# Optimization experiments

Hardware: AMD Instinct MI355X
Metric: run time of the kernel (lower is better)

Reference implementation:

```python
import jax, jax.numpy as jnp
import numpy as np

C = 256      # n_embd
H = 16       # n_head
HS = C // H  # head_size = 16
B = 64
T = 256      # <= block_size
LN_EPS = 1e-5


def _layer_norm(x, g, b):
    mu = jnp.mean(x, axis=-1, keepdims=True)
    var = jnp.mean((x - mu) ** 2, axis=-1, keepdims=True)
    return (x - mu) * jax.lax.rsqrt(var + LN_EPS) * g + b


def setup_inputs() -> dict:
    key = jax.random.key(0)
    ks = jax.random.split(key, 10)
    s_in = 1.0 / np.sqrt(C)
    s_ff = 1.0 / np.sqrt(4 * C)
    return {
        "x": jax.random.normal(ks[0], (B, T, C), dtype=jnp.float32),
        # per-head Q/K/V weights, stacked: [H, C, HS] (no bias, as in Head)
        "Wq": jax.random.normal(ks[1], (H, C, HS), dtype=jnp.float32) * s_in,
        "Wk": jax.random.normal(ks[2], (H, C, HS), dtype=jnp.float32) * s_in,
        "Wv": jax.random.normal(ks[3], (H, C, HS), dtype=jnp.float32) * s_in,
        "Wp": jax.random.normal(ks[4], (C, C), dtype=jnp.float32) * s_in,
        "bp": jnp.zeros((C,), dtype=jnp.float32),
        "W1": jax.random.normal(ks[5], (C, 4 * C), dtype=jnp.float32) * s_in,
        "b1": jnp.zeros((4 * C,), dtype=jnp.float32),
        "W2": jax.random.normal(ks[6], (4 * C, C), dtype=jnp.float32) * s_ff,
        "b2": jnp.zeros((C,), dtype=jnp.float32),
        "g1": jnp.ones((C,), dtype=jnp.float32),
        "be1": jnp.zeros((C,), dtype=jnp.float32),
        "g2": jnp.ones((C,), dtype=jnp.float32),
        "be2": jnp.zeros((C,), dtype=jnp.float32),
    }


def reference(x, Wq, Wk, Wv, Wp, bp, W1, b1, W2, b2, g1, be1, g2, be2):
    Bx, Tx, Cx = x.shape
    h = _layer_norm(x, g1, be1)
    # per-head projections: [B, H, T, HS]
    q = jnp.einsum('btc,hcd->bhtd', h, Wq)
    k = jnp.einsum('btc,hcd->bhtd', h, Wk)
    v = jnp.einsum('btc,hcd->bhtd', h, Wv)
    # NOTE: original scales by C**-0.5 with C = n_embd, NOT head_size
    scale = 1.0 / np.sqrt(Cx)
    scores = jnp.einsum('bhtd,bhsd->bhts', q, k) * scale
    causal = jnp.tril(jnp.ones((Tx, Tx), dtype=bool))
    scores = jnp.where(causal, scores, -jnp.inf)
    wei = jax.nn.softmax(scores, axis=-1)  # dropout = identity (eval)
    attn = jnp.einsum('bhts,bhsd->bhtd', wei, v)
    # concat heads in order -> [B, T, C]
    attn = attn.transpose(0, 2, 1, 3).reshape(Bx, Tx, Cx)
    attn = attn @ Wp + bp
    x = x + attn
    h2 = _layer_norm(x, g2, be2)
    ffn = jax.nn.gelu(h2 @ W1 + b1, approximate=False) @ W2 + b2
    return x + ffn


if __name__ == "__main__":
    out = reference(**setup_inputs())
    print(out.shape, out.dtype)
```

## Files before the change

kernel.cpp:

```cpp
#include <hip/hip_runtime.h>
#include <hip/hip_bf16.h>

typedef __attribute__((ext_vector_type(8))) short short8;
typedef __attribute__((ext_vector_type(4))) float f32x4;
typedef __attribute__((ext_vector_type(16))) float f32x16;

__device__ __forceinline__ unsigned short f2bf(float f) {
    unsigned u = __float_as_uint(f);
    unsigned r = (u + 0x7fffu + ((u >> 16) & 1u)) >> 16;
    return (unsigned short)r;
}

__device__ __forceinline__ float fast_gelu(float v) {
    float y  = 0.7978845608f * v * (1.0f + 0.044715f * v * v);
    float ay = fabsf(y);
    float e  = __expf(2.0f * ay);
    float th = 1.0f - 2.0f / (e + 1.0f);
    th = __builtin_copysignf(th, y);
    return 0.5f * v * (1.0f + th);
}

__device__ __forceinline__ void gload16(const unsigned short* g, unsigned short* l) {
    __builtin_amdgcn_global_load_lds(
        (const __attribute__((address_space(1))) unsigned int*)g,
        (__attribute__((address_space(3))) unsigned int*)l,
        16, 0, 0);
}

__global__ __launch_bounds__(256) void ln_kernel(
    const float* __restrict__ xin, const float* __restrict__ gw,
    const float* __restrict__ bw, unsigned short* __restrict__ out)
{
    int row  = blockIdx.x * 4 + (threadIdx.x >> 6);
    int lane = threadIdx.x & 63;
    const float4 v = *reinterpret_cast<const float4*>(xin + (size_t)row * 256 + lane * 4);
    float s  = v.x + v.y + v.z + v.w;
    float sq = v.x*v.x + v.y*v.y + v.z*v.z + v.w*v.w;
#pragma unroll
    for (int m = 1; m < 64; m <<= 1) { s += __shfl_xor(s, m); sq += __shfl_xor(sq, m); }
    float mean = s * (1.0f/256.0f);
    float var  = sq * (1.0f/256.0f) - mean*mean;
    float rstd = rsqrtf(var + 1e-5f);
    const float4 g4 = *reinterpret_cast<const float4*>(gw + lane*4);
    const float4 b4 = *reinterpret_cast<const float4*>(bw + lane*4);
    ushort4 o;
    o.x = f2bf((v.x-mean)*rstd*g4.x + b4.x);
    o.y = f2bf((v.y-mean)*rstd*g4.y + b4.y);
    o.z = f2bf((v.z-mean)*rstd*g4.z + b4.z);
    o.w = f2bf((v.w-mean)*rstd*g4.w + b4.w);
    *reinterpret_cast<ushort4*>(out + (size_t)row*256 + lane*4) = o;
}

__global__ __launch_bounds__(256) void prep_fused(
    const float* __restrict__ Wq, const float* __restrict__ Wk,
    const float* __restrict__ Wv, const float* __restrict__ Wp,
    const float* __restrict__ W1, const float* __restrict__ W2,
    unsigned short* __restrict__ WqkvT, unsigned short* __restrict__ WpT,
    unsigned short* __restrict__ W1T, unsigned short* __restrict__ W2T)
{
    __shared__ float smem[4096];
    const int bid = blockIdx.x, t = threadIdx.x;
    if (bid < 576) {
        const float* W; unsigned short* WT; int N, K, tile0;
        if (bid < 64)       { W = Wp; WT = WpT; N = 256;  K = 256;  tile0 = bid; }
        else if (bid < 320) { W = W1; WT = W1T; N = 1024; K = 256;  tile0 = bid - 64; }
        else                { W = W2; WT = W2T; N = 256;  K = 1024; tile0 = bid - 320; }
        int ntx = N >> 5;
        int bx = tile0 % ntx, by = tile0 / ntx;
        int c0 = bx*32, r0 = by*32;
        int tx = t & 31, ty = t >> 5;
#pragma unroll
        for (int i = 0; i < 4; ++i)
            smem[(ty + i*8)*33 + tx] = W[(size_t)(r0 + ty + i*8)*N + c0 + tx];
        __syncthreads();
#pragma unroll
        for (int i = 0; i < 4; ++i)
            WT[(size_t)(c0 + ty + i*8)*K + r0 + tx] = f2bf(smem[tx*33 + ty + i*8]);
    } else {
        int pb = bid - 576;
        int proj = pb >> 4, hh = pb & 15;
        const float* W = (proj == 0) ? Wq : ((proj == 1) ? Wk : Wv);
        float scale = (proj == 0) ? 0.0625f : 1.0f;
        const float4* src = reinterpret_cast<const float4*>(W + hh*4096);
#pragma unroll
        for (int i = 0; i < 4; ++i) {
            float4 v4 = src[t + i*256];
            *reinterpret_cast<float4*>(&smem[(t + i*256)*4]) = v4;
        }
        __syncthreads();
        int d = t >> 4, cp = (t & 15) * 16;
        unsigned short obuf[16];
#pragma unroll
        for (int i = 0; i < 16; ++i)
            obuf[i] = f2bf(smem[(cp + i)*16 + d] * scale);
        unsigned short* dst = WqkvT + (size_t)(proj*256 + hh*16 + d)*256 + cp;
        *reinterpret_cast<ushort4*>(dst)      = *reinterpret_cast<ushort4*>(&obuf[0]);
        *reinterpret_cast<ushort4*>(dst + 4)  = *reinterpret_cast<ushort4*>(&obuf[4]);
        *reinterpret_cast<ushort4*>(dst + 8)  = *reinterpret_cast<ushort4*>(&obuf[8]);
        *reinterpret_cast<ushort4*>(dst + 12) = *reinterpret_cast<ushort4*>(&obuf[12]);
    }
}

template<int NBX>
__device__ __forceinline__ void swz_bid(int& bx, int& by) {
    int nwg = gridDim.x;
    int bid = blockIdx.x;
    int vid = (bid & 7) * (nwg >> 3) + (bid >> 3);
    bx = vid % NBX;
    by = vid / NBX;
}

template<int BM, int BN, int K>
__device__ __forceinline__ void gemm_core(
    const unsigned short* __restrict__ A, const unsigned short* __restrict__ BT,
    int bx, int by, f32x4 (&acc)[BM/32][BN/32])
{
    constexpr int FM = BM/32, FN = BN/32, NT = K/32;
    __shared__ unsigned short As[2][BM*32];
    __shared__ unsigned short Bs[2][BN*32];
    const int tid = threadIdx.x, lane = tid & 63, wid = tid >> 6;
    const int wr = (wid >> 1) * (BM/2), wc = (wid & 1) * (BN/2);
    const int c16 = lane & 15, g16 = lane >> 4;
    const int lr = lane >> 2, lq = lane & 3;

#pragma unroll
    for (int m = 0; m < FM; ++m)
#pragma unroll
        for (int n = 0; n < FN; ++n) acc[m][n] = f32x4{0.f, 0.f, 0.f, 0.f};

    const unsigned short* a0 = A  + (size_t)(by*BM + lr)*K + lq*8;
    const unsigned short* b0 = BT + (size_t)(bx*BN + lr)*K + lq*8;

    auto stage = [&](int buf, int t) {
        int k0 = t * 32;
#pragma unroll
        for (int i = 0; i < BM/64; ++i) {
            int ch = wid*(BM/64) + i;
            gload16(a0 + (size_t)ch*16*K + k0, &As[buf][ch*512]);
        }
#pragma unroll
        for (int i = 0; i < BN/64; ++i) {
            int ch = wid*(BN/64) + i;
            gload16(b0 + (size_t)ch*16*K + k0, &Bs[buf][ch*512]);
        }
    };

    auto compute = [&](int buf) {
        short8 af[FM], bf[FN];
#pragma unroll
        for (int m = 0; m < FM; ++m)
            af[m] = *reinterpret_cast<const short8*>(&As[buf][(wr + m*16 + c16)*32 + g16*8]);
#pragma unroll
        for (int n = 0; n < FN; ++n)
            bf[n] = *reinterpret_cast<const short8*>(&Bs[buf][(wc + n*16 + c16)*32 + g16*8]);
#pragma unroll
        for (int m = 0; m < FM; ++m)
#pragma unroll
            for (int n = 0; n < FN; ++n)
                acc[m][n] = __builtin_amdgcn_mfma_f32_16x16x32_bf16(af[m], bf[n], acc[m][n], 0, 0, 0);
    };

    stage(0, 0);
    __syncthreads();
    int cur = 0;
    for (int t = 0; t < NT-1; ++t) {
        stage(cur ^ 1, t + 1);
        compute(cur);
        __syncthreads();
        cur ^= 1;
    }
    compute(cur);
}

__global__ __launch_bounds__(256) void gemm_qkv(
    const unsigned short* __restrict__ A, const unsigned short* __restrict__ BT,
    unsigned short* __restrict__ qb, unsigned short* __restrict__ kb,
    unsigned short* __restrict__ vtb)
{
    int bx, by; swz_bid<6>(bx, by);
    f32x4 acc[4][4];
    gemm_core<128, 128, 256>(A, BT, bx, by, acc);
    const int lane = threadIdx.x & 63, wid = threadIdx.x >> 6;
    const int c16 = lane & 15, g16 = lane >> 4;
    const int wr = (wid >> 1) * 64, wc = (wid & 1) * 64;
#pragma unroll
    for (int m = 0; m < 4; ++m)
#pragma unroll
    for (int n = 0; n < 4; ++n)
#pragma unroll
    for (int j = 0; j < 4; ++j) {
        int row = by*128 + wr + m*16 + g16*4 + j;
        int col = bx*128 + wc + n*16 + c16;
        int proj = col >> 8, hh = (col >> 4) & 15, dd = col & 15;
        int b = row >> 8, t = row & 255;
        unsigned short val = f2bf(acc[m][n][j]);
        size_t bh = (size_t)(b*16 + hh);
        if (proj == 0)      qb[(bh*256 + t)*16 + dd] = val;
        else if (proj == 1) kb[(bh*256 + t)*16 + dd] = val;
        else                vtb[(bh*16 + dd)*256 + t] = val;
    }
}

__global__ __launch_bounds__(256) void gemm_wp(
    const unsigned short* __restrict__ A, const unsigned short* __restrict__ BT,
    const float* __restrict__ bp, const float* __restrict__ x, float* __restrict__ x2)
{
    int bx, by; swz_bid<2>(bx, by);
    f32x4 acc[2][4];
    gemm_core<64, 128, 256>(A, BT, bx, by, acc);
    const int lane = threadIdx.x & 63, wid = threadIdx.x >> 6;
    const int c16 = lane & 15, g16 = lane >> 4;
    const int wr = (wid >> 1) * 32, wc = (wid & 1) * 64;
#pragma unroll
    for (int m = 0; m < 2; ++m)
#pragma unroll
    for (int n = 0; n < 4; ++n)
#pragma unroll
    for (int j = 0; j < 4; ++j) {
        int row = by*64 + wr + m*16 + g16*4 + j;
        int col = bx*128 + wc + n*16 + c16;
        size_t idx = (size_t)row*256 + col;
        x2[idx] = acc[m][n][j] + bp[col] + x[idx];
    }
}

__global__ __launch_bounds__(256) void gemm_ffn1(
    const unsigned short* __restrict__ A, const unsigned short* __restrict__ BT,
    const float* __restrict__ b1, unsigned short* __restrict__ ffh)
{
    int bx, by; swz_bid<8>(bx, by);
    f32x4 acc[4][4];
    gemm_core<128, 128, 256>(A, BT, bx, by, acc);
    const int lane = threadIdx.x & 63, wid = threadIdx.x >> 6;
    const int c16 = lane & 15, g16 = lane >> 4;
    const int wr = (wid >> 1) * 64, wc = (wid & 1) * 64;
#pragma unroll
    for (int m = 0; m < 4; ++m)
#pragma unroll
    for (int n = 0; n < 4; ++n)
#pragma unroll
    for (int j = 0; j < 4; ++j) {
        int row = by*128 + wr + m*16 + g16*4 + j;
        int col = bx*128 + wc + n*16 + c16;
        float v = acc[m][n][j] + b1[col];
        ffh[(size_t)row*1024 + col] = f2bf(fast_gelu(v));
    }
}

__global__ __launch_bounds__(256) void gemm_ffn2(
    const unsigned short* __restrict__ A, const unsigned short* __restrict__ BT,
    const float* __restrict__ b2, const float* __restrict__ x2, float* __restrict__ out)
{
    int bx, by; swz_bid<2>(bx, by);
    f32x4 acc[2][4];
    gemm_core<64, 128, 1024>(A, BT, bx, by, acc);
    const int lane = threadIdx.x & 63, wid = threadIdx.x >> 6;
    const int c16 = lane & 15, g16 = lane >> 4;
    const int wr = (wid >> 1) * 32, wc = (wid & 1) * 64;
#pragma unroll
    for (int m = 0; m < 2; ++m)
#pragma unroll
    for (int n = 0; n < 4; ++n)
#pragma unroll
    for (int j = 0; j < 4; ++j) {
        int row = by*64 + wr + m*16 + g16*4 + j;
        int col = bx*128 + wc + n*16 + c16;
        size_t idx = (size_t)row*256 + col;
        out[idx] = acc[m][n][j] + b2[col] + x2[idx];
    }
}

__global__ __launch_bounds__(256) void attn_kernel(
    const unsigned short* __restrict__ qb, const unsigned short* __restrict__ kb,
    const unsigned short* __restrict__ vtb, unsigned short* __restrict__ ao)
{
    const int bid  = blockIdx.x;
    const int half = bid & 1, h = (bid >> 1) & 15, b = bid >> 5;
    const int tid  = threadIdx.x;
    const int w    = tid >> 6, lane = tid & 63;
    const int l31  = lane & 31, hi = lane >> 5;
    const int chunk = half*4 + w;
    const int t0    = chunk * 32;
    const unsigned short* qh = qb  + (size_t)(b*16 + h) * 4096;
    const unsigned short* kh = kb  + (size_t)(b*16 + h) * 4096;
    const unsigned short* vh = vtb + (size_t)(b*16 + h) * 4096;

    short8 qf = *reinterpret_cast<const short8*>(qh + (size_t)(t0 + l31)*16 + hi*8);

    f32x16 zf, pv;
#pragma unroll
    for (int i = 0; i < 16; ++i) { zf[i] = 0.f; pv[i] = 0.f; }
    float sum = 0.f;
    const int dref = l31 & 15;

    for (int tt = 0; tt <= chunk; ++tt) {
        short8 kf = *reinterpret_cast<const short8*>(kh + (size_t)(tt*32 + l31)*16 + hi*8);
        f32x16 S = __builtin_amdgcn_mfma_f32_32x32x16_bf16(kf, qf, zf, 0, 0, 0);

        float p[16];
#pragma unroll
        for (int r = 0; r < 16; ++r) {
            float pe = __expf(S[r]);
            if (tt == chunk) {
                int s_local = (r & 3) + 8*(r >> 2) + 4*hi;
                pe = (s_local <= l31) ? pe : 0.f;
            }
            p[r] = pe;
            sum += pe;
        }

        unsigned qd[8], xd[8];
#pragma unroll
        for (int i = 0; i < 8; ++i) {
            unsigned rr;
            asm("v_cvt_pk_bf16_f32 %0, %1, %2" : "=v"(rr) : "v"(p[2*i]), "v"(p[2*i+1]));
            qd[i] = rr;
        }
#pragma unroll
        for (int i = 0; i < 8; ++i) xd[i] = (unsigned)__shfl_xor((int)qd[i], 32);

        int4 flo, fhi;
        flo.x = hi ? (int)xd[2] : (int)qd[0];
        flo.y = hi ? (int)xd[3] : (int)qd[1];
        flo.z = hi ? (int)qd[2] : (int)xd[0];
        flo.w = hi ? (int)qd[3] : (int)xd[1];
        fhi.x = hi ? (int)xd[6] : (int)qd[4];
        fhi.y = hi ? (int)xd[7] : (int)qd[5];
        fhi.z = hi ? (int)qd[6] : (int)xd[4];
        fhi.w = hi ? (int)qd[7] : (int)xd[5];
        short8 plo = __builtin_bit_cast(short8, flo);
        short8 phi = __builtin_bit_cast(short8, fhi);

        short8 vf0 = *reinterpret_cast<const short8*>(vh + (size_t)dref*256 + tt*32 + hi*8);
        short8 vf1 = *reinterpret_cast<const short8*>(vh + (size_t)dref*256 + tt*32 + 16 + hi*8);
        pv = __builtin_amdgcn_mfma_f32_32x32x16_bf16(vf0, plo, pv, 0, 0, 0);
        pv = __builtin_amdgcn_mfma_f32_32x32x16_bf16(vf1, phi, pv, 0, 0, 0);
    }

    sum += __shfl_xor(sum, 32);
    float rinv = 1.0f / sum;

    unsigned o0, o1, o2, o3;
    {
        float a0 = pv[0]*rinv, a1 = pv[1]*rinv, a2 = pv[2]*rinv, a3 = pv[3]*rinv;
        float a4 = pv[4]*rinv, a5 = pv[5]*rinv, a6 = pv[6]*rinv, a7 = pv[7]*rinv;
        asm("v_cvt_pk_bf16_f32 %0, %1, %2" : "=v"(o0) : "v"(a0), "v"(a1));
        asm("v_cvt_pk_bf16_f32 %0, %1, %2" : "=v"(o1) : "v"(a2), "v"(a3));
        asm("v_cvt_pk_bf16_f32 %0, %1, %2" : "=v"(o2) : "v"(a4), "v"(a5));
        asm("v_cvt_pk_bf16_f32 %0, %1, %2" : "=v"(o3) : "v"(a6), "v"(a7));
    }
    unsigned short* orow = ao + (size_t)(b*256 + t0 + l31)*256 + h*16;
    uint2 s01 = {o0, o1}, s23 = {o2, o3};
    *reinterpret_cast<uint2*>(orow + hi*4)     = s01;
    *reinterpret_cast<uint2*>(orow + 8 + hi*4) = s23;
}

extern "C" void kernel_launch(void* const* d_in, const int* in_sizes, int n_in,
                              void* d_out, int out_size, void* d_ws, size_t ws_size,
                              hipStream_t stream)
{
    const float* x   = (const float*)d_in[0];
    const float* Wq  = (const float*)d_in[1];
    const float* Wk  = (const float*)d_in[2];
    const float* Wv  = (const float*)d_in[3];
    const float* Wp  = (const float*)d_in[4];
    const float* bp  = (const float*)d_in[5];
    const float* W1  = (const float*)d_in[6];
    const float* b1  = (const float*)d_in[7];
    const float* W2  = (const float*)d_in[8];
    const float* b2  = (const float*)d_in[9];
    const float* g1  = (const float*)d_in[10];
    const float* be1 = (const float*)d_in[11];
    const float* g2  = (const float*)d_in[12];
    const float* be2 = (const float*)d_in[13];
    float* out = (float*)d_out;

    char* ws = (char*)d_ws;
    unsigned short* h1    = (unsigned short*)(ws);
    unsigned short* WqkvT = (unsigned short*)(ws +  8388608);
    unsigned short* WpT   = (unsigned short*)(ws +  8781824);
    unsigned short* W1T   = (unsigned short*)(ws +  8912896);
    unsigned short* W2T   = (unsigned short*)(ws +  9437184);
    unsigned short* qb    = (unsigned short*)(ws +  9961472);
    unsigned short* kb    = (unsigned short*)(ws + 18350080);
    unsigned short* vtb   = (unsigned short*)(ws + 26738688);
    unsigned short* ao    = (unsigned short*)(ws + 35127296);
    unsigned short* ffh   = qb;
    float*          x2    = (float*)(ws + 43515904);
    unsigned short* h2    = (unsigned short*)(ws + 60293120);

    prep_fused<<<624, 256, 0, stream>>>(Wq, Wk, Wv, Wp, W1, W2, WqkvT, WpT, W1T, W2T);
    ln_kernel<<<4096, 256, 0, stream>>>(x, g1, be1, h1);
    gemm_qkv<<<768, 256, 0, stream>>>(h1, WqkvT, qb, kb, vtb);
    attn_kernel<<<2048, 256, 0, stream>>>(qb, kb, vtb, ao);
    gemm_wp<<<512, 256, 0, stream>>>(ao, WpT, bp, x, x2);
    ln_kernel<<<4096, 256, 0, stream>>>(x2, g2, be2, h2);
    gemm_ffn1<<<1024, 256, 0, stream>>>(h2, W1T, b1, ffh);
    gemm_ffn2<<<512, 256, 0, stream>>>(ffh, W2T, b2, x2, out);
}
```

Before: 126.8 us.

## Fuse LN2 into Wp GEMM epilogue, merge LN1 into prep, widen output GEMMs

LN1 is folded into the weight-prep launch as extra blocks. The Wp projection GEMM now uses 512-thread blocks covering full 256-column rows, so its epilogue can compute the LayerNorm2 statistics through shuffles and shared memory and write h2 directly. This removes a separate kernel launch and a full re-read of x2. The FFN2 GEMM uses the same 64x256 full-row tiling with 8 waves, which halves the block count to 256 and may underfill the GPU's compute units.

```diff
diff --git a/kernel.cpp b/kernel.cpp
--- a/kernel.cpp
+++ b/kernel.cpp
@@ -27,39 +27,38 @@
         16, 0, 0);
 }
 
-__global__ __launch_bounds__(256) void ln_kernel(
-    const float* __restrict__ xin, const float* __restrict__ gw,
-    const float* __restrict__ bw, unsigned short* __restrict__ out)
-{
-    int row  = blockIdx.x * 4 + (threadIdx.x >> 6);
-    int lane = threadIdx.x & 63;
-    const float4 v = *reinterpret_cast<const float4*>(xin + (size_t)row * 256 + lane * 4);
-    float s  = v.x + v.y + v.z + v.w;
-    float sq = v.x*v.x + v.y*v.y + v.z*v.z + v.w*v.w;
-#pragma unroll
-    for (int m = 1; m < 64; m <<= 1) { s += __shfl_xor(s, m); sq += __shfl_xor(sq, m); }
-    float mean = s * (1.0f/256.0f);
-    float var  = sq * (1.0f/256.0f) - mean*mean;
-    float rstd = rsqrtf(var + 1e-5f);
-    const float4 g4 = *reinterpret_cast<const float4*>(gw + lane*4);
-    const float4 b4 = *reinterpret_cast<const float4*>(bw + lane*4);
-    ushort4 o;
-    o.x = f2bf((v.x-mean)*rstd*g4.x + b4.x);
-    o.y = f2bf((v.y-mean)*rstd*g4.y + b4.y);
-    o.z = f2bf((v.z-mean)*rstd*g4.z + b4.z);
-    o.w = f2bf((v.w-mean)*rstd*g4.w + b4.w);
-    *reinterpret_cast<ushort4*>(out + (size_t)row*256 + lane*4) = o;
-}
-
-__global__ __launch_bounds__(256) void prep_fused(
+__global__ __launch_bounds__(256) void prep_ln1(
     const float* __restrict__ Wq, const float* __restrict__ Wk,
     const float* __restrict__ Wv, const float* __restrict__ Wp,
     const float* __restrict__ W1, const float* __restrict__ W2,
     unsigned short* __restrict__ WqkvT, unsigned short* __restrict__ WpT,
-    unsigned short* __restrict__ W1T, unsigned short* __restrict__ W2T)
+    unsigned short* __restrict__ W1T, unsigned short* __restrict__ W2T,
+    const float* __restrict__ xin, const float* __restrict__ gw,
+    const float* __restrict__ bw, unsigned short* __restrict__ h1)
 {
     __shared__ float smem[4096];
     const int bid = blockIdx.x, t = threadIdx.x;
+    if (bid >= 624) {
+        int row  = (bid - 624) * 4 + (t >> 6);
+        int lane = t & 63;
+        const float4 v = *reinterpret_cast<const float4*>(xin + (size_t)row * 256 + lane * 4);
+        float s  = v.x + v.y + v.z + v.w;
+        float sq = v.x*v.x + v.y*v.y + v.z*v.z + v.w*v.w;
+#pragma unroll
+        for (int m = 1; m < 64; m <<= 1) { s += __shfl_xor(s, m); sq += __shfl_xor(sq, m); }
+        float mean = s * (1.0f/256.0f);
+        float var  = sq * (1.0f/256.0f) - mean*mean;
+        float rstd = rsqrtf(var + 1e-5f);
+        const float4 g4 = *reinterpret_cast<const float4*>(gw + lane*4);
+        const float4 b4 = *reinterpret_cast<const float4*>(bw + lane*4);
+        ushort4 o;
+        o.x = f2bf((v.x-mean)*rstd*g4.x + b4.x);
+        o.y = f2bf((v.y-mean)*rstd*g4.y + b4.y);
+        o.z = f2bf((v.z-mean)*rstd*g4.z + b4.z);
+        o.w = f2bf((v.w-mean)*rstd*g4.w + b4.w);
+        *reinterpret_cast<ushort4*>(h1 + (size_t)row*256 + lane*4) = o;
+        return;
+    }
     if (bid < 576) {
         const float* W; unsigned short* WT; int N, K, tile0;
         if (bid < 64)       { W = Wp; WT = WpT; N = 256;  K = 256;  tile0 = bid; }
@@ -153,6 +152,68 @@
 #pragma unroll
         for (int n = 0; n < FN; ++n)
             bf[n] = *reinterpret_cast<const short8*>(&Bs[buf][(wc + n*16 + c16)*32 + g16*8]);
+#pragma unroll
+        for (int m = 0; m < FM; ++m)
+#pragma unroll
+            for (int n = 0; n < FN; ++n)
+                acc[m][n] = __builtin_amdgcn_mfma_f32_16x16x32_bf16(af[m], bf[n], acc[m][n], 0, 0, 0);
+    };
+
+    stage(0, 0);
+    __syncthreads();
+    int cur = 0;
+    for (int t = 0; t < NT-1; ++t) {
+        stage(cur ^ 1, t + 1);
+        compute(cur);
+        __syncthreads();
+        cur ^= 1;
+    }
+    compute(cur);
+}
+
+template<int BM, int BN, int K>
+__device__ __forceinline__ void gemm_core8(
+    const unsigned short* __restrict__ A, const unsigned short* __restrict__ BT,
+    int by, f32x4 (&acc)[BM/32][BN/64])
+{
+    constexpr int FM = BM/32, FN = BN/64, NT = K/32;
+    constexpr int NCHA = BM/16, NCH = BM/16 + BN/16;
+    constexpr int NR = (NCH + 7) / 8;
+    __shared__ unsigned short As[2][BM*32];
+    __shared__ unsigned short Bs[2][BN*32];
+    const int tid = threadIdx.x, lane = tid & 63, wid = tid >> 6;
+    const int wm = wid >> 2, wn = wid & 3;
+    const int c16 = lane & 15, g16 = lane >> 4;
+    const int lr = lane >> 2, lq = lane & 3;
+
+#pragma unroll
+    for (int m = 0; m < FM; ++m)
+#pragma unroll
+        for (int n = 0; n < FN; ++n) acc[m][n] = f32x4{0.f, 0.f, 0.f, 0.f};
+
+    const unsigned short* a0 = A  + (size_t)(by*BM + lr)*K + lq*8;
+    const unsigned short* b0 = BT + (size_t)lr*K + lq*8;
+
+    auto stage = [&](int buf, int t) {
+        int k0 = t * 32;
+#pragma unroll
+        for (int i = 0; i < NR; ++i) {
+            int ch = i*8 + wid;
+            if (ch < NCHA)
+                gload16(a0 + (size_t)ch*16*K + k0, &As[buf][ch*512]);
+            else if (ch < NCH)
+                gload16(b0 + (size_t)(ch-NCHA)*16*K + k0, &Bs[buf][(ch-NCHA)*512]);
+        }
+    };
+
+    auto compute = [&](int buf) {
+        short8 af[FM], bf[FN];
+#pragma unroll
+        for (int m = 0; m < FM; ++m)
+            af[m] = *reinterpret_cast<const short8*>(&As[buf][(wm*(BM/2) + m*16 + c16)*32 + g16*8]);
+#pragma unroll
+        for (int n = 0; n < FN; ++n)
+            bf[n] = *reinterpret_cast<const short8*>(&Bs[buf][(wn*(BN/4) + n*16 + c16)*32 + g16*8]);
 #pragma unroll
         for (int m = 0; m < FM; ++m)
 #pragma unroll
@@ -201,26 +262,71 @@
     }
 }
 
-__global__ __launch_bounds__(256) void gemm_wp(
+__global__ __launch_bounds__(512) void gemm_wp_ln(
     const unsigned short* __restrict__ A, const unsigned short* __restrict__ BT,
-    const float* __restrict__ bp, const float* __restrict__ x, float* __restrict__ x2)
-{
-    int bx, by; swz_bid<2>(bx, by);
+    const float* __restrict__ bp, const float* __restrict__ x,
+    const float* __restrict__ g2, const float* __restrict__ be2,
+    float* __restrict__ x2, unsigned short* __restrict__ h2)
+{
+    int bx, by; swz_bid<1>(bx, by);
     f32x4 acc[2][4];
-    gemm_core<64, 128, 256>(A, BT, bx, by, acc);
-    const int lane = threadIdx.x & 63, wid = threadIdx.x >> 6;
+    gemm_core8<64, 256, 256>(A, BT, by, acc);
+
+    __shared__ float rs[64][4];
+    __shared__ float rq[64][4];
+    const int tid = threadIdx.x, lane = tid & 63, wid = tid >> 6;
     const int c16 = lane & 15, g16 = lane >> 4;
-    const int wr = (wid >> 1) * 32, wc = (wid & 1) * 64;
+    const int wm = wid >> 2, wn = wid & 3;
+
+    float vv[2][4][4];
 #pragma unroll
     for (int m = 0; m < 2; ++m)
 #pragma unroll
     for (int n = 0; n < 4; ++n)
 #pragma unroll
     for (int j = 0; j < 4; ++j) {
-        int row = by*64 + wr + m*16 + g16*4 + j;
-        int col = bx*128 + wc + n*16 + c16;
+        int row = by*64 + wm*32 + m*16 + g16*4 + j;
+        int col = wn*64 + n*16 + c16;
         size_t idx = (size_t)row*256 + col;
-        x2[idx] = acc[m][n][j] + bp[col] + x[idx];
+        float v = acc[m][n][j] + bp[col] + x[idx];
+        vv[m][n][j] = v;
+        x2[idx] = v;
+    }
+#pragma unroll
+    for (int m = 0; m < 2; ++m)
+#pragma unroll
+    for (int j = 0; j < 4; ++j) {
+        float ps = vv[m][0][j] + vv[m][1][j] + vv[m][2][j] + vv[m][3][j];
+        float pq = vv[m][0][j]*vv[m][0][j] + vv[m][1][j]*vv[m][1][j]
+                 + vv[m][2][j]*vv[m][2][j] + vv[m][3][j]*vv[m][3][j];
+#pragma unroll
+        for (int mask = 1; mask < 16; mask <<= 1) {
+            ps += __shfl_xor(ps, mask);
+            pq += __shfl_xor(pq, mask);
+        }
+        if (c16 == 0) {
+            int r = wm*32 + m*16 + g16*4 + j;
+            rs[r][wn] = ps;
+            rq[r][wn] = pq;
+        }
+    }
+    __syncthreads();
+#pragma unroll
+    for (int m = 0; m < 2; ++m)
+#pragma unroll
+    for (int j = 0; j < 4; ++j) {
+        int r = wm*32 + m*16 + g16*4 + j;
+        float s = rs[r][0] + rs[r][1] + rs[r][2] + rs[r][3];
+        float q = rq[r][0] + rq[r][1] + rq[r][2] + rq[r][3];
+        float mean = s * (1.0f/256.0f);
+        float var  = q * (1.0f/256.0f) - mean*mean;
+        float rstd = rsqrtf(var + 1e-5f);
+        int row = by*64 + r;
+#pragma unroll
+        for (int n = 0; n < 4; ++n) {
+            int col = wn*64 + n*16 + c16;
+            h2[(size_t)row*256 + col] = f2bf((vv[m][n][j]-mean)*rstd*g2[col] + be2[col]);
+        }
     }
 }
 
@@ -247,24 +353,24 @@
     }
 }
 
-__global__ __launch_bounds__(256) void gemm_ffn2(
+__global__ __launch_bounds__(512) void gemm_ffn2(
     const unsigned short* __restrict__ A, const unsigned short* __restrict__ BT,
     const float* __restrict__ b2, const float* __restrict__ x2, float* __restrict__ out)
 {
-    int bx, by; swz_bid<2>(bx, by);
+    int bx, by; swz_bid<1>(bx, by);
     f32x4 acc[2][4];
-    gemm_core<64, 128, 1024>(A, BT, bx, by, acc);
+    gemm_core8<64, 256, 1024>(A, BT, by, acc);
     const int lane = threadIdx.x & 63, wid = threadIdx.x >> 6;
     const int c16 = lane & 15, g16 = lane >> 4;
-    const int wr = (wid >> 1) * 32, wc = (wid & 1) * 64;
+    const int wm = wid >> 2, wn = wid & 3;
 #pragma unroll
     for (int m = 0; m < 2; ++m)
 #pragma unroll
     for (int n = 0; n < 4; ++n)
 #pragma unroll
     for (int j = 0; j < 4; ++j) {
-        int row = by*64 + wr + m*16 + g16*4 + j;
-        int col = bx*128 + wc + n*16 + c16;
+        int row = by*64 + wm*32 + m*16 + g16*4 + j;
+        int col = wn*64 + n*16 + c16;
         size_t idx = (size_t)row*256 + col;
         out[idx] = acc[m][n][j] + b2[col] + x2[idx];
     }
@@ -389,12 +495,11 @@
     float*          x2    = (float*)(ws + 43515904);
     unsigned short* h2    = (unsigned short*)(ws + 60293120);
 
-    prep_fused<<<624, 256, 0, stream>>>(Wq, Wk, Wv, Wp, W1, W2, WqkvT, WpT, W1T, W2T);
-    ln_kernel<<<4096, 256, 0, stream>>>(x, g1, be1, h1);
+    prep_ln1<<<4720, 256, 0, stream>>>(Wq, Wk, Wv, Wp, W1, W2,
+                                       WqkvT, WpT, W1T, W2T, x, g1, be1, h1);
     gemm_qkv<<<768, 256, 0, stream>>>(h1, WqkvT, qb, kb, vtb);
     attn_kernel<<<2048, 256, 0, stream>>>(qb, kb, vtb, ao);
-    gemm_wp<<<512, 256, 0, stream>>>(ao, WpT, bp, x, x2);
-    ln_kernel<<<4096, 256, 0, stream>>>(x2, g2, be2, h2);
+    gemm_wp_ln<<<256, 512, 0, stream>>>(ao, WpT, bp, x, g2, be2, x2, h2);
     gemm_ffn1<<<1024, 256, 0, stream>>>(h2, W1T, b1, ffh);
-    gemm_ffn2<<<512, 256, 0, stream>>>(ffh, W2T, b2, x2, out);
-}
+    gemm_ffn2<<<256, 512, 0, stream>>>(ffh, W2T, b2, x2, out);
+}
```

After: 115.4 us. -9.0%, faster.
